# Kernel tuning notes

Hardware: AMD Instinct MI355X
Metric: run time of the kernel (lower is better)

The kernel has to match this reference:

```python
import jax, jax.numpy as jnp
import numpy as np

SEQ, D_IN, D_OUT = 8192, 1024, 1024


def setup_inputs() -> dict:
    key = jax.random.key(0)
    kx, kq, kk, kv = jax.random.split(key, 4)
    x = jax.random.normal(kx, (SEQ, D_IN), dtype=jnp.float32)
    # original uses torch.rand (uniform [0,1)) for parameter init
    WQ = jax.random.uniform(kq, (D_IN, D_OUT), dtype=jnp.float32)
    WK = jax.random.uniform(kk, (D_IN, D_OUT), dtype=jnp.float32)
    WV = jax.random.uniform(kv, (D_IN, D_OUT), dtype=jnp.float32)
    return {"x": x, "WQ": WQ, "WK": WK, "WV": WV}


def reference(x, WQ, WK, WV):
    # [seq, d_out] projections
    q = x @ WQ
    k = x @ WK
    v = x @ WV
    # [seq, seq] raw attention scores
    attn_score = q @ k.T
    # NOTE: source module computes softmax(attn_score/sqrt(d)) into attn_wt
    # but then multiplies the RAW scores by values (attn_score @ values).
    # attn_wt is dead code w.r.t. the output, so it is omitted here.
    context_vct = attn_score @ v  # [seq, d_out]
    return context_vct
```

## Files before the change

kernel.cpp:

```cpp
#include <hip/hip_runtime.h>
#include <hip/hip_bf16.h>
#include <stdint.h>
#include <stddef.h>

#define SEQ  8192
#define DIN  1024
#define DOUT 1024

typedef __hip_bfloat16 bf16;
typedef short bf16x8 __attribute__((ext_vector_type(8)));
typedef float f32x4  __attribute__((ext_vector_type(4)));

#define GLOAD_LDS16(gptr, lptr)                                                     \
  __builtin_amdgcn_global_load_lds(                                                 \
      (const __attribute__((address_space(1))) void*)(gptr),                        \
      (__attribute__((address_space(3))) void*)(lptr), 16, 0, 0)

__device__ inline void store_out(float* p, float v) { *p = v; }
__device__ inline void store_out(bf16* p, float v) { *p = __float2bfloat16(v); }
__device__ inline short bfbits(float f) { bf16 b = __float2bfloat16(f); return *(short*)&b; }
__device__ inline float bf2f(short u) {
  unsigned v = ((unsigned)(unsigned short)u) << 16;
  return __uint_as_float(v);
}

template <typename OutT>
__device__ __forceinline__ void gemm128_body(
    const bf16* __restrict__ A, const bf16* __restrict__ B, OutT* __restrict__ C,
    int bx, int by, int K, int lda, int ldb, int ldc, bf16* As, bf16* Bs)
{
  const int lane = threadIdx.x & 63;
  const int wave = threadIdx.x >> 6;
  const int m0 = by * 128, n0 = bx * 128;

  const int sR = lane >> 3;
  const int sC = (lane & 7) ^ sR;
  const bf16* gA = A + (size_t)(m0 + sR) * lda + sC * 8;
  const bf16* gB = B + (size_t)(n0 + sR) * ldb + sC * 8;

  f32x4 acc[4][4];
#pragma unroll
  for (int i = 0; i < 4; ++i)
#pragma unroll
    for (int j = 0; j < 4; ++j)
      acc[i][j] = (f32x4){0.f, 0.f, 0.f, 0.f};

  const int wr = wave >> 1, wc = wave & 1;
  const int mW = wr * 64, nW = wc * 64;
  const int fragRow = lane & 15;
  const int quad = lane >> 4;

  auto stage = [&](int kt, int buf) {
    bf16* dA = As + buf * (128 * 64);
    bf16* dB = Bs + buf * (128 * 64);
#pragma unroll
    for (int t = 0; t < 4; ++t) {
      const int R = (t * 4 + wave) * 8;
      GLOAD_LDS16(gA + (size_t)R * lda + kt, &dA[R * 64]);
      GLOAD_LDS16(gB + (size_t)R * ldb + kt, &dB[R * 64]);
    }
  };

  const int nT = K >> 6;
  stage(0, 0);
  for (int kt = 0; kt < nT; ++kt) {
    const int buf = kt & 1;
    if (kt + 1 < nT) {
      stage((kt + 1) << 6, buf ^ 1);
      asm volatile("s_waitcnt vmcnt(8)" ::: "memory");
    } else {
      asm volatile("s_waitcnt vmcnt(0)" ::: "memory");
    }
    asm volatile("s_barrier" ::: "memory");

    const bf16* Ab = As + buf * (128 * 64);
    const bf16* Bb = Bs + buf * (128 * 64);
    bf16x8 afr[2][4], bfr[2][4];
#pragma unroll
    for (int s = 0; s < 2; ++s) {
      const int cw = s * 4 + quad;
#pragma unroll
      for (int i = 0; i < 4; ++i) {
        const int ra = mW + i * 16 + fragRow;
        afr[s][i] = *(const bf16x8*)&Ab[ra * 64 + ((cw ^ (ra & 7)) << 3)];
        const int rb = nW + i * 16 + fragRow;
        bfr[s][i] = *(const bf16x8*)&Bb[rb * 64 + ((cw ^ (rb & 7)) << 3)];
      }
    }
    asm volatile("s_waitcnt lgkmcnt(0)" ::: "memory");
    asm volatile("s_barrier" ::: "memory");

#pragma unroll
    for (int s = 0; s < 2; ++s)
#pragma unroll
      for (int i = 0; i < 4; ++i)
#pragma unroll
        for (int j = 0; j < 4; ++j)
          acc[i][j] = __builtin_amdgcn_mfma_f32_16x16x32_bf16(afr[s][i], bfr[s][j], acc[i][j], 0, 0, 0);
  }

  const int cCol  = lane & 15;
  const int cRow4 = quad * 4;
#pragma unroll
  for (int i = 0; i < 4; ++i)
#pragma unroll
    for (int j = 0; j < 4; ++j) {
      const int row = m0 + mW + i * 16 + cRow4;
      const int col = n0 + nW + j * 16 + cCol;
#pragma unroll
      for (int r = 0; r < 4; ++r)
        store_out(&C[(size_t)(row + r) * ldc + col], acc[i][j][r]);
    }
}

template <typename OutT>
__device__ __forceinline__ void gemm64_body(
    const bf16* __restrict__ A, const bf16* __restrict__ B, OutT* __restrict__ C,
    int bx, int by, int K, int lda, int ldb, int ldc, bf16* As, bf16* Bs)
{
  const int lane = threadIdx.x & 63;
  const int wave = threadIdx.x >> 6;
  const int m0 = by * 64, n0 = bx * 64;

  const int sR = lane >> 3;
  const int sC = (lane & 7) ^ sR;
  const bf16* gA = A + (size_t)(m0 + sR) * lda + sC * 8;
  const bf16* gB = B + (size_t)(n0 + sR) * ldb + sC * 8;

  f32x4 acc[2][2];
#pragma unroll
  for (int i = 0; i < 2; ++i)
#pragma unroll
    for (int j = 0; j < 2; ++j)
      acc[i][j] = (f32x4){0.f, 0.f, 0.f, 0.f};

  const int wr = wave >> 1, wc = wave & 1;
  const int mW = wr * 32, nW = wc * 32;
  const int fragRow = lane & 15;
  const int quad = lane >> 4;

  auto stage = [&](int kt, int buf) {
    bf16* dA = As + buf * (64 * 64);
    bf16* dB = Bs + buf * (64 * 64);
#pragma unroll
    for (int t = 0; t < 2; ++t) {
      const int R = (t * 4 + wave) * 8;
      GLOAD_LDS16(gA + (size_t)R * lda + kt, &dA[R * 64]);
      GLOAD_LDS16(gB + (size_t)R * ldb + kt, &dB[R * 64]);
    }
  };

  const int nT = K >> 6;
  stage(0, 0);
  for (int kt = 0; kt < nT; ++kt) {
    const int buf = kt & 1;
    if (kt + 1 < nT) {
      stage((kt + 1) << 6, buf ^ 1);
      asm volatile("s_waitcnt vmcnt(4)" ::: "memory");
    } else {
      asm volatile("s_waitcnt vmcnt(0)" ::: "memory");
    }
    asm volatile("s_barrier" ::: "memory");

    const bf16* Ab = As + buf * (64 * 64);
    const bf16* Bb = Bs + buf * (64 * 64);
    bf16x8 afr[2][2], bfr[2][2];
#pragma unroll
    for (int s = 0; s < 2; ++s) {
      const int cw = s * 4 + quad;
#pragma unroll
      for (int i = 0; i < 2; ++i) {
        const int ra = mW + i * 16 + fragRow;
        afr[s][i] = *(const bf16x8*)&Ab[ra * 64 + ((cw ^ (ra & 7)) << 3)];
        const int rb = nW + i * 16 + fragRow;
        bfr[s][i] = *(const bf16x8*)&Bb[rb * 64 + ((cw ^ (rb & 7)) << 3)];
      }
    }
    asm volatile("s_waitcnt lgkmcnt(0)" ::: "memory");
    asm volatile("s_barrier" ::: "memory");

#pragma unroll
    for (int s = 0; s < 2; ++s)
#pragma unroll
      for (int i = 0; i < 2; ++i)
#pragma unroll
        for (int j = 0; j < 2; ++j)
          acc[i][j] = __builtin_amdgcn_mfma_f32_16x16x32_bf16(afr[s][i], bfr[s][j], acc[i][j], 0, 0, 0);
  }

  const int cCol  = lane & 15;
  const int cRow4 = quad * 4;
#pragma unroll
  for (int i = 0; i < 2; ++i)
#pragma unroll
    for (int j = 0; j < 2; ++j) {
      const int row = m0 + mW + i * 16 + cRow4;
      const int col = n0 + nW + j * 16 + cCol;
#pragma unroll
      for (int r = 0; r < 4; ++r)
        store_out(&C[(size_t)(row + r) * ldc + col], acc[i][j][r]);
    }
}

__global__ __launch_bounds__(256) void g_p1(
    const bf16* __restrict__ xT, const bf16* __restrict__ WQb,
    const bf16* __restrict__ WKb, bf16* __restrict__ part, bf16* __restrict__ P1)
{
  __shared__ bf16 sm[4 * 128 * 64];
  const int b = blockIdx.x;
  if (b < 512) {
    const int z = b & 7;
    const int r = b >> 3;
    const bf16* Az = xT + (size_t)z * 1024;
    gemm128_body<bf16>(Az, Az, part + ((size_t)z << 20),
                       r & 7, r >> 3, 1024, 8192, 8192, 1024,
                       sm, sm + 2 * 128 * 64);
  } else {
    const int p = b - 512;
    gemm64_body<bf16>(WQb, WKb, P1, p & 15, p >> 4, 1024, 1024, 1024, 1024,
                      sm, sm + 2 * 64 * 64);
  }
}

__global__ __launch_bounds__(256) void gemm128_f32(
    const bf16* __restrict__ A, const bf16* __restrict__ B, float* __restrict__ C,
    int K, int lda, int ldb, int ldc)
{
  __shared__ bf16 sm[4 * 128 * 64];
  const int id = blockIdx.x;
  const int by = ((id & 7) << 3) | ((id >> 3) & 7);
  const int bx = id >> 6;
  gemm128_body<float>(A, B, C, bx, by, K, lda, ldb, ldc, sm, sm + 2 * 128 * 64);
}

__global__ __launch_bounds__(256) void gemm64_bf(
    const bf16* __restrict__ A, const bf16* __restrict__ B, bf16* __restrict__ C,
    int K, int lda, int ldb, int ldc)
{
  __shared__ bf16 sm[4 * 64 * 64];
  gemm64_body<bf16>(A, B, C, blockIdx.x, blockIdx.y, K, lda, ldb, ldc,
                    sm, sm + 2 * 64 * 64);
}

__global__ __launch_bounds__(256) void prep_all(
    const float* __restrict__ x, const float* __restrict__ WQ,
    const float* __restrict__ WK, const float* __restrict__ WV,
    bf16* __restrict__ xb, bf16* __restrict__ xTb,
    bf16* __restrict__ WQb, bf16* __restrict__ WKb, bf16* __restrict__ WVTb)
{
  __shared__ bf16 t[128][68];
  int b = blockIdx.x;

  if (b < 5120) {
    const size_t i = ((size_t)b * 256 + threadIdx.x) * 8;
    const float* src; bf16* dst;
    if (i < 8388608)      { src = x  + i;           dst = xb  + i; }
    else if (i < 9437184) { src = WQ + (i - 8388608); dst = WQb + (i - 8388608); }
    else                  { src = WK + (i - 9437184); dst = WKb + (i - 9437184); }
    const float4 f0 = *(const float4*)src;
    const float4 f1 = *(const float4*)(src + 4);
    bf16x8 o;
    o[0] = bfbits(f0.x); o[1] = bfbits(f0.y); o[2] = bfbits(f0.z); o[3] = bfbits(f0.w);
    o[4] = bfbits(f1.x); o[5] = bfbits(f1.y); o[6] = bfbits(f1.z); o[7] = bfbits(f1.w);
    *(bf16x8*)dst = o;
    return;
  }

  b -= 5120;
  const float* src; bf16* dst; int ldOut, tr, tc;
  if (b < 1024) { src = x;  dst = xTb;  ldOut = SEQ; tr = b >> 4; tc = b & 15; }
  else { b -= 1024; src = WV; dst = WVTb; ldOut = DIN; tr = b >> 4; tc = b & 15; }
  const int r0 = tr * 128, c0 = tc * 64;

#pragma unroll
  for (int p = 0; p < 8; ++p) {
    const int q = threadIdx.x + p * 256;
    const int r = q >> 4, c4 = (q & 15) * 4;
    const float4 f = *(const float4*)&src[(size_t)(r0 + r) * DIN + c0 + c4];
    short4 s4;
    s4.x = bfbits(f.x); s4.y = bfbits(f.y); s4.z = bfbits(f.z); s4.w = bfbits(f.w);
    *(short4*)&t[r][c4] = s4;
  }
  __syncthreads();

#pragma unroll
  for (int p = 0; p < 4; ++p) {
    const int h = threadIdx.x + p * 256;
    const int c = h >> 4, seg = h & 15;
    bf16x8 o;
#pragma unroll
    for (int i = 0; i < 8; ++i)
      o[i] = *(const short*)&t[seg * 8 + i][c];
    *(bf16x8*)&dst[(size_t)(c0 + c) * ldOut + r0 + seg * 8] = o;
  }
}

__global__ void reduce8(const bf16* __restrict__ part, bf16* __restrict__ out, int S)
{
  const int i = blockIdx.x * blockDim.x + threadIdx.x;
  const size_t base = (size_t)i * 8;
  float s[8] = {0.f, 0.f, 0.f, 0.f, 0.f, 0.f, 0.f, 0.f};
  for (int z = 0; z < S; ++z) {
    bf16x8 v = *(const bf16x8*)&part[((size_t)z << 20) + base];
#pragma unroll
    for (int r = 0; r < 8; ++r) s[r] += bf2f(v[r]);
  }
  bf16x8 o;
#pragma unroll
  for (int r = 0; r < 8; ++r) o[r] = bfbits(s[r]);
  *(bf16x8*)&out[base] = o;
}

extern "C" void kernel_launch(void* const* d_in, const int* in_sizes, int n_in,
                              void* d_out, int out_size, void* d_ws, size_t ws_size,
                              hipStream_t stream)
{
  const float* x  = (const float*)d_in[0];
  const float* WQ = (const float*)d_in[1];
  const float* WK = (const float*)d_in[2];
  const float* WV = (const float*)d_in[3];
  float* out = (float*)d_out;

  char* ws = (char*)d_ws;
  size_t off = 0;
  auto alloc = [&](size_t bytes) -> void* {
    void* p = ws + off;
    off += (bytes + 255) & ~(size_t)255;
    return p;
  };

  const size_t xBytes = (size_t)SEQ * DIN * sizeof(bf16);
  const size_t wBytes = (size_t)DIN * DOUT * sizeof(bf16);
  const int S = 8;

  bf16* xb   = (bf16*)alloc(xBytes);
  bf16* xTb  = (bf16*)alloc(xBytes);
  bf16* WQb  = (bf16*)alloc(wBytes);
  bf16* WKb  = (bf16*)alloc(wBytes);
  bf16* WVTb = (bf16*)alloc(wBytes);
  bf16* Gb   = (bf16*)alloc(wBytes);
  bf16* P1b  = (bf16*)alloc(wBytes);
  bf16* Utb  = (bf16*)alloc(wBytes);
  bf16* WpTb = (bf16*)alloc(wBytes);
  bf16* part = (bf16*)alloc((size_t)S * wBytes);

  prep_all<<<dim3(6272), 256, 0, stream>>>(x, WQ, WK, WV, xb, xTb, WQb, WKb, WVTb);

  g_p1<<<dim3(768), 256, 0, stream>>>(xTb, WQb, WKb, part, P1b);

  reduce8<<<dim3(512), 256, 0, stream>>>(part, Gb, S);

  gemm64_bf<<<dim3(16, 16), 256, 0, stream>>>(WVTb, Gb, Utb, 1024, 1024, 1024, 1024);
  gemm64_bf<<<dim3(16, 16), 256, 0, stream>>>(Utb, P1b, WpTb, 1024, 1024, 1024, 1024);

  gemm128_f32<<<dim3(512), 256, 0, stream>>>(xb, WpTb, out, 1024, 1024, 1024, DOUT);
}
```

Baseline: 164.5 us.

## Fuse WQ·WKᵀ product into prep kernel and emit xb during transpose

The separate elementwise bf16 conversion pass over x, WQ and WK is removed. The row-major bf16 copy of x is now written inside the transpose blocks that already read x. The WQ·WKᵀ product (P1) is computed directly from fp32 inputs by new blocks in the prep kernel, converting to bf16 while staging into shared memory. The x^T x partial GEMM kernel no longer carries the P1 blocks. This cuts an extra full read of x and an intermediate write and read of the weights. In exchange, the new P1 path has no async loads or double buffering, and the xb stores are short4-sized and less coalesced.

```diff
diff --git a/kernel.cpp b/kernel.cpp
--- a/kernel.cpp
+++ b/kernel.cpp
@@ -202,24 +202,107 @@
     }
 }
 
-__global__ __launch_bounds__(256) void g_p1(
-    const bf16* __restrict__ xT, const bf16* __restrict__ WQb,
-    const bf16* __restrict__ WKb, bf16* __restrict__ part, bf16* __restrict__ P1)
+__device__ __forceinline__ void p1_body(
+    const float* __restrict__ A, const float* __restrict__ B, bf16* __restrict__ C,
+    int bx, int by, bf16* As, bf16* Bs)
+{
+  const int tid  = threadIdx.x;
+  const int lane = tid & 63;
+  const int wave = tid >> 6;
+  const int m0 = by * 64, n0 = bx * 64;
+
+  const int sRow = tid >> 2;
+  const int sJ   = (tid & 3) << 1;
+
+  f32x4 acc[2][2];
+#pragma unroll
+  for (int i = 0; i < 2; ++i)
+#pragma unroll
+    for (int j = 0; j < 2; ++j)
+      acc[i][j] = (f32x4){0.f, 0.f, 0.f, 0.f};
+
+  const int wr = wave >> 1, wc = wave & 1;
+  const int mW = wr * 32, nW = wc * 32;
+  const int fragRow = lane & 15;
+  const int quad = lane >> 4;
+
+  const float* gA = A + (size_t)(m0 + sRow) * 1024;
+  const float* gB = B + (size_t)(n0 + sRow) * 1024;
+
+  for (int kt = 0; kt < 16; ++kt) {
+    const int k0 = kt << 6;
+    float4 ra[2][2], rb[2][2];
+#pragma unroll
+    for (int u = 0; u < 2; ++u) {
+      const int c = k0 + ((sJ + u) << 3);
+      ra[u][0] = *(const float4*)&gA[c];
+      ra[u][1] = *(const float4*)&gA[c + 4];
+      rb[u][0] = *(const float4*)&gB[c];
+      rb[u][1] = *(const float4*)&gB[c + 4];
+    }
+    __syncthreads();
+#pragma unroll
+    for (int u = 0; u < 2; ++u) {
+      bf16x8 pa, pb;
+      pa[0] = bfbits(ra[u][0].x); pa[1] = bfbits(ra[u][0].y);
+      pa[2] = bfbits(ra[u][0].z); pa[3] = bfbits(ra[u][0].w);
+      pa[4] = bfbits(ra[u][1].x); pa[5] = bfbits(ra[u][1].y);
+      pa[6] = bfbits(ra[u][1].z); pa[7] = bfbits(ra[u][1].w);
+      pb[0] = bfbits(rb[u][0].x); pb[1] = bfbits(rb[u][0].y);
+      pb[2] = bfbits(rb[u][0].z); pb[3] = bfbits(rb[u][0].w);
+      pb[4] = bfbits(rb[u][1].x); pb[5] = bfbits(rb[u][1].y);
+      pb[6] = bfbits(rb[u][1].z); pb[7] = bfbits(rb[u][1].w);
+      *(bf16x8*)&As[sRow * 72 + (sJ + u) * 8] = pa;
+      *(bf16x8*)&Bs[sRow * 72 + (sJ + u) * 8] = pb;
+    }
+    __syncthreads();
+
+    bf16x8 afr[2][2], bfr[2][2];
+#pragma unroll
+    for (int s = 0; s < 2; ++s) {
+      const int cw = s * 4 + quad;
+#pragma unroll
+      for (int i = 0; i < 2; ++i) {
+        const int rr = mW + i * 16 + fragRow;
+        afr[s][i] = *(const bf16x8*)&As[rr * 72 + cw * 8];
+        const int cc = nW + i * 16 + fragRow;
+        bfr[s][i] = *(const bf16x8*)&Bs[cc * 72 + cw * 8];
+      }
+    }
+#pragma unroll
+    for (int s = 0; s < 2; ++s)
+#pragma unroll
+      for (int i = 0; i < 2; ++i)
+#pragma unroll
+        for (int j = 0; j < 2; ++j)
+          acc[i][j] = __builtin_amdgcn_mfma_f32_16x16x32_bf16(afr[s][i], bfr[s][j], acc[i][j], 0, 0, 0);
+  }
+
+  const int cCol  = lane & 15;
+  const int cRow4 = quad * 4;
+#pragma unroll
+  for (int i = 0; i < 2; ++i)
+#pragma unroll
+    for (int j = 0; j < 2; ++j) {
+      const int row = m0 + mW + i * 16 + cRow4;
+      const int col = n0 + nW + j * 16 + cCol;
+#pragma unroll
+      for (int r = 0; r < 4; ++r)
+        store_out(&C[(size_t)(row + r) * 1024 + col], acc[i][j][r]);
+    }
+}
+
+__global__ __launch_bounds__(256) void g_G(
+    const bf16* __restrict__ xT, bf16* __restrict__ part)
 {
   __shared__ bf16 sm[4 * 128 * 64];
   const int b = blockIdx.x;
-  if (b < 512) {
-    const int z = b & 7;
-    const int r = b >> 3;
-    const bf16* Az = xT + (size_t)z * 1024;
-    gemm128_body<bf16>(Az, Az, part + ((size_t)z << 20),
-                       r & 7, r >> 3, 1024, 8192, 8192, 1024,
-                       sm, sm + 2 * 128 * 64);
-  } else {
-    const int p = b - 512;
-    gemm64_body<bf16>(WQb, WKb, P1, p & 15, p >> 4, 1024, 1024, 1024, 1024,
-                      sm, sm + 2 * 64 * 64);
-  }
+  const int z = b & 7;
+  const int r = b >> 3;
+  const bf16* Az = xT + (size_t)z * 1024;
+  gemm128_body<bf16>(Az, Az, part + ((size_t)z << 20),
+                     r & 7, r >> 3, 1024, 8192, 8192, 1024,
+                     sm, sm + 2 * 128 * 64);
 }
 
 __global__ __launch_bounds__(256) void gemm128_f32(
@@ -246,30 +329,21 @@
     const float* __restrict__ x, const float* __restrict__ WQ,
     const float* __restrict__ WK, const float* __restrict__ WV,
     bf16* __restrict__ xb, bf16* __restrict__ xTb,
-    bf16* __restrict__ WQb, bf16* __restrict__ WKb, bf16* __restrict__ WVTb)
-{
-  __shared__ bf16 t[128][68];
+    bf16* __restrict__ WVTb, bf16* __restrict__ P1)
+{
+  __shared__ __align__(16) bf16 sm[2 * 64 * 72];
   int b = blockIdx.x;
 
-  if (b < 5120) {
-    const size_t i = ((size_t)b * 256 + threadIdx.x) * 8;
-    const float* src; bf16* dst;
-    if (i < 8388608)      { src = x  + i;           dst = xb  + i; }
-    else if (i < 9437184) { src = WQ + (i - 8388608); dst = WQb + (i - 8388608); }
-    else                  { src = WK + (i - 9437184); dst = WKb + (i - 9437184); }
-    const float4 f0 = *(const float4*)src;
-    const float4 f1 = *(const float4*)(src + 4);
-    bf16x8 o;
-    o[0] = bfbits(f0.x); o[1] = bfbits(f0.y); o[2] = bfbits(f0.z); o[3] = bfbits(f0.w);
-    o[4] = bfbits(f1.x); o[5] = bfbits(f1.y); o[6] = bfbits(f1.z); o[7] = bfbits(f1.w);
-    *(bf16x8*)dst = o;
+  if (b < 256) {
+    p1_body(WQ, WK, P1, b & 15, b >> 4, sm, sm + 64 * 72);
     return;
   }
-
-  b -= 5120;
-  const float* src; bf16* dst; int ldOut, tr, tc;
-  if (b < 1024) { src = x;  dst = xTb;  ldOut = SEQ; tr = b >> 4; tc = b & 15; }
-  else { b -= 1024; src = WV; dst = WVTb; ldOut = DIN; tr = b >> 4; tc = b & 15; }
+  b -= 256;
+
+  bf16 (*t)[68] = (bf16(*)[68])sm;
+  const float* src; bf16* dst; int ldOut, tr, tc; bool isX;
+  if (b < 1024) { src = x;  dst = xTb;  ldOut = SEQ; tr = b >> 4; tc = b & 15; isX = true; }
+  else { b -= 1024; src = WV; dst = WVTb; ldOut = DIN; tr = b >> 4; tc = b & 15; isX = false; }
   const int r0 = tr * 128, c0 = tc * 64;
 
 #pragma unroll
@@ -280,6 +354,7 @@
     short4 s4;
     s4.x = bfbits(f.x); s4.y = bfbits(f.y); s4.z = bfbits(f.z); s4.w = bfbits(f.w);
     *(short4*)&t[r][c4] = s4;
+    if (isX) *(short4*)&xb[(size_t)(r0 + r) * DIN + c0 + c4] = s4;
   }
   __syncthreads();
 
@@ -335,8 +410,6 @@
 
   bf16* xb   = (bf16*)alloc(xBytes);
   bf16* xTb  = (bf16*)alloc(xBytes);
-  bf16* WQb  = (bf16*)alloc(wBytes);
-  bf16* WKb  = (bf16*)alloc(wBytes);
   bf16* WVTb = (bf16*)alloc(wBytes);
   bf16* Gb   = (bf16*)alloc(wBytes);
   bf16* P1b  = (bf16*)alloc(wBytes);
@@ -344,9 +417,9 @@
   bf16* WpTb = (bf16*)alloc(wBytes);
   bf16* part = (bf16*)alloc((size_t)S * wBytes);
 
-  prep_all<<<dim3(6272), 256, 0, stream>>>(x, WQ, WK, WV, xb, xTb, WQb, WKb, WVTb);
-
-  g_p1<<<dim3(768), 256, 0, stream>>>(xTb, WQb, WKb, part, P1b);
+  prep_all<<<dim3(1408), 256, 0, stream>>>(x, WQ, WK, WV, xb, xTb, WVTb, P1b);
+
+  g_G<<<dim3(512), 256, 0, stream>>>(xTb, part);
 
   reduce8<<<dim3(512), 256, 0, stream>>>(part, Gb, S);
 
```

Measured after the change: 168.2 us. +2.2%, slower.

## Exploit Gram matrix symmetry and fuse x conversion into transpose pass

Applied to the files above, without the earlier changes.

The Gram matrix G = x^T x is now computed only for the 36 upper-triangular 128x128 tiles, with split-K partials reduced in a new kernel that also writes the mirrored transpose tile through swizzled LDS. The x bf16 cast is folded into the transposing prep pass so x is read once instead of twice, and the P1 and Ut GEMMs are merged into one launch. This cuts G-GEMM work by nearly half and removes a launch. The cost is a serialized reduction over only 36 blocks and a triangular grid of 288 blocks, which may underfill the GPU.

```diff
diff --git a/kernel.cpp b/kernel.cpp
--- a/kernel.cpp
+++ b/kernel.cpp
@@ -22,6 +22,12 @@
 __device__ inline float bf2f(short u) {
   unsigned v = ((unsigned)(unsigned short)u) << 16;
   return __uint_as_float(v);
+}
+
+__device__ inline void tri_map(int t, int& ti, int& tj) {
+  int a = 0, rem = t;
+  while (rem >= 8 - a) { rem -= 8 - a; ++a; }
+  ti = a; tj = a + rem;
 }
 
 template <typename OutT>
@@ -202,24 +208,89 @@
     }
 }
 
-__global__ __launch_bounds__(256) void g_p1(
-    const bf16* __restrict__ xT, const bf16* __restrict__ WQb,
-    const bf16* __restrict__ WKb, bf16* __restrict__ part, bf16* __restrict__ P1)
+__global__ __launch_bounds__(256) void g_G(
+    const bf16* __restrict__ xT, bf16* __restrict__ part)
 {
   __shared__ bf16 sm[4 * 128 * 64];
   const int b = blockIdx.x;
-  if (b < 512) {
-    const int z = b & 7;
-    const int r = b >> 3;
-    const bf16* Az = xT + (size_t)z * 1024;
-    gemm128_body<bf16>(Az, Az, part + ((size_t)z << 20),
-                       r & 7, r >> 3, 1024, 8192, 8192, 1024,
-                       sm, sm + 2 * 128 * 64);
+  const int z = b & 7;
+  const int t = b >> 3;
+  int ti, tj; tri_map(t, ti, tj);
+  const bf16* Az = xT + (size_t)z * 1024;
+  gemm128_body<bf16>(Az + (size_t)ti * 128 * 8192,
+                     Az + (size_t)tj * 128 * 8192,
+                     part + ((size_t)(z * 36 + t)) * 16384,
+                     0, 0, 1024, 8192, 8192, 128,
+                     sm, sm + 2 * 128 * 64);
+}
+
+__global__ __launch_bounds__(256) void reduceT(
+    const bf16* __restrict__ part, bf16* __restrict__ G)
+{
+  __shared__ bf16 red[128 * 128];
+  const int t = blockIdx.x;
+  int ti, tj; tri_map(t, ti, tj);
+  const int tid = threadIdx.x;
+  const size_t base = (size_t)t * 16384;
+  const bool diag = (ti == tj);
+
+#pragma unroll
+  for (int it = 0; it < 8; ++it) {
+    const int flat = it * 256 + tid;
+    const int row = flat >> 4, chunk = flat & 15;
+    float a[8] = {0.f, 0.f, 0.f, 0.f, 0.f, 0.f, 0.f, 0.f};
+    for (int z = 0; z < 8; ++z) {
+      bf16x8 v = *(const bf16x8*)&part[(size_t)z * 36 * 16384 + base + row * 128 + chunk * 8];
+#pragma unroll
+      for (int r = 0; r < 8; ++r) a[r] += bf2f(v[r]);
+    }
+    bf16x8 o;
+#pragma unroll
+    for (int r = 0; r < 8; ++r) o[r] = bfbits(a[r]);
+    *(bf16x8*)&G[(size_t)(ti * 128 + row) * 1024 + tj * 128 + chunk * 8] = o;
+    if (!diag)
+      *(bf16x8*)&red[row * 128 + ((chunk ^ (row >> 3)) << 3)] = o;
+  }
+  if (diag) return;
+  __syncthreads();
+
+#pragma unroll
+  for (int it = 0; it < 8; ++it) {
+    const int flat = it * 256 + tid;
+    const int c = flat >> 4, seg = flat & 15;
+    const int swz = ((((c >> 3) ^ seg)) << 3) + (c & 7);
+    bf16x8 o;
+#pragma unroll
+    for (int i = 0; i < 8; ++i)
+      o[i] = *(const short*)&red[(seg * 8 + i) * 128 + swz];
+    *(bf16x8*)&G[(size_t)(tj * 128 + c) * 1024 + ti * 128 + seg * 8] = o;
+  }
+}
+
+__global__ __launch_bounds__(256) void g_ut_p1(
+    const bf16* __restrict__ WVT, const bf16* __restrict__ G,
+    const bf16* __restrict__ WQb, const bf16* __restrict__ WKb,
+    bf16* __restrict__ Ut, bf16* __restrict__ P1)
+{
+  __shared__ bf16 sm[4 * 64 * 64];
+  int b = blockIdx.x;
+  if (b < 256) {
+    gemm64_body<bf16>(WQb, WKb, P1, b & 15, b >> 4, 1024, 1024, 1024, 1024,
+                      sm, sm + 2 * 64 * 64);
   } else {
-    const int p = b - 512;
-    gemm64_body<bf16>(WQb, WKb, P1, p & 15, p >> 4, 1024, 1024, 1024, 1024,
+    b -= 256;
+    gemm64_body<bf16>(WVT, G, Ut, b & 15, b >> 4, 1024, 1024, 1024, 1024,
                       sm, sm + 2 * 64 * 64);
   }
+}
+
+__global__ __launch_bounds__(256) void gemm64_bf(
+    const bf16* __restrict__ A, const bf16* __restrict__ B, bf16* __restrict__ C,
+    int K, int lda, int ldb, int ldc)
+{
+  __shared__ bf16 sm[4 * 64 * 64];
+  gemm64_body<bf16>(A, B, C, blockIdx.x, blockIdx.y, K, lda, ldb, ldc,
+                    sm, sm + 2 * 64 * 64);
 }
 
 __global__ __launch_bounds__(256) void gemm128_f32(
@@ -233,15 +304,6 @@
   gemm128_body<float>(A, B, C, bx, by, K, lda, ldb, ldc, sm, sm + 2 * 128 * 64);
 }
 
-__global__ __launch_bounds__(256) void gemm64_bf(
-    const bf16* __restrict__ A, const bf16* __restrict__ B, bf16* __restrict__ C,
-    int K, int lda, int ldb, int ldc)
-{
-  __shared__ bf16 sm[4 * 64 * 64];
-  gemm64_body<bf16>(A, B, C, blockIdx.x, blockIdx.y, K, lda, ldb, ldc,
-                    sm, sm + 2 * 64 * 64);
-}
-
 __global__ __launch_bounds__(256) void prep_all(
     const float* __restrict__ x, const float* __restrict__ WQ,
     const float* __restrict__ WK, const float* __restrict__ WV,
@@ -251,12 +313,11 @@
   __shared__ bf16 t[128][68];
   int b = blockIdx.x;
 
-  if (b < 5120) {
-    const size_t i = ((size_t)b * 256 + threadIdx.x) * 8;
+  if (b >= 1152) {
+    const size_t i = ((size_t)(b - 1152) * 256 + threadIdx.x) * 8;
     const float* src; bf16* dst;
-    if (i < 8388608)      { src = x  + i;           dst = xb  + i; }
-    else if (i < 9437184) { src = WQ + (i - 8388608); dst = WQb + (i - 8388608); }
-    else                  { src = WK + (i - 9437184); dst = WKb + (i - 9437184); }
+    if (i < 1048576) { src = WQ + i;             dst = WQb + i; }
+    else             { src = WK + (i - 1048576); dst = WKb + (i - 1048576); }
     const float4 f0 = *(const float4*)src;
     const float4 f1 = *(const float4*)(src + 4);
     bf16x8 o;
@@ -266,10 +327,9 @@
     return;
   }
 
-  b -= 5120;
-  const float* src; bf16* dst; int ldOut, tr, tc;
-  if (b < 1024) { src = x;  dst = xTb;  ldOut = SEQ; tr = b >> 4; tc = b & 15; }
-  else { b -= 1024; src = WV; dst = WVTb; ldOut = DIN; tr = b >> 4; tc = b & 15; }
+  const float* src; bf16* dst; int ldOut, tr, tc; bool isX;
+  if (b < 1024) { src = x;  dst = xTb;  ldOut = SEQ; tr = b >> 4; tc = b & 15; isX = true; }
+  else { b -= 1024; src = WV; dst = WVTb; ldOut = DIN; tr = b >> 4; tc = b & 15; isX = false; }
   const int r0 = tr * 128, c0 = tc * 64;
 
 #pragma unroll
@@ -280,6 +340,7 @@
     short4 s4;
     s4.x = bfbits(f.x); s4.y = bfbits(f.y); s4.z = bfbits(f.z); s4.w = bfbits(f.w);
     *(short4*)&t[r][c4] = s4;
+    if (isX) *(short4*)&xb[(size_t)(r0 + r) * DIN + c0 + c4] = s4;
   }
   __syncthreads();
 
@@ -293,22 +354,6 @@
       o[i] = *(const short*)&t[seg * 8 + i][c];
     *(bf16x8*)&dst[(size_t)(c0 + c) * ldOut + r0 + seg * 8] = o;
   }
-}
-
-__global__ void reduce8(const bf16* __restrict__ part, bf16* __restrict__ out, int S)
-{
-  const int i = blockIdx.x * blockDim.x + threadIdx.x;
-  const size_t base = (size_t)i * 8;
-  float s[8] = {0.f, 0.f, 0.f, 0.f, 0.f, 0.f, 0.f, 0.f};
-  for (int z = 0; z < S; ++z) {
-    bf16x8 v = *(const bf16x8*)&part[((size_t)z << 20) + base];
-#pragma unroll
-    for (int r = 0; r < 8; ++r) s[r] += bf2f(v[r]);
-  }
-  bf16x8 o;
-#pragma unroll
-  for (int r = 0; r < 8; ++r) o[r] = bfbits(s[r]);
-  *(bf16x8*)&out[base] = o;
 }
 
 extern "C" void kernel_launch(void* const* d_in, const int* in_sizes, int n_in,
@@ -331,7 +376,6 @@
 
   const size_t xBytes = (size_t)SEQ * DIN * sizeof(bf16);
   const size_t wBytes = (size_t)DIN * DOUT * sizeof(bf16);
-  const int S = 8;
 
   bf16* xb   = (bf16*)alloc(xBytes);
   bf16* xTb  = (bf16*)alloc(xBytes);
@@ -342,15 +386,16 @@
   bf16* P1b  = (bf16*)alloc(wBytes);
   bf16* Utb  = (bf16*)alloc(wBytes);
   bf16* WpTb = (bf16*)alloc(wBytes);
-  bf16* part = (bf16*)alloc((size_t)S * wBytes);
-
-  prep_all<<<dim3(6272), 256, 0, stream>>>(x, WQ, WK, WV, xb, xTb, WQb, WKb, WVTb);
-
-  g_p1<<<dim3(768), 256, 0, stream>>>(xTb, WQb, WKb, part, P1b);
-
-  reduce8<<<dim3(512), 256, 0, stream>>>(part, Gb, S);
-
-  gemm64_bf<<<dim3(16, 16), 256, 0, stream>>>(WVTb, Gb, Utb, 1024, 1024, 1024, 1024);
+  bf16* part = (bf16*)alloc((size_t)8 * 36 * 16384 * sizeof(bf16));
+
+  prep_all<<<dim3(2176), 256, 0, stream>>>(x, WQ, WK, WV, xb, xTb, WQb, WKb, WVTb);
+
+  g_G<<<dim3(288), 256, 0, stream>>>(xTb, part);
+
+  reduceT<<<dim3(36), 256, 0, stream>>>(part, Gb);
+
+  g_ut_p1<<<dim3(512), 256, 0, stream>>>(WVTb, Gb, WQb, WKb, Utb, P1b);
+
   gemm64_bf<<<dim3(16, 16), 256, 0, stream>>>(Utb, P1b, WpTb, 1024, 1024, 1024, 1024);
 
   gemm128_f32<<<dim3(512), 256, 0, stream>>>(xb, WpTb, out, 1024, 1024, 1024, DOUT);
```

Measured after the change: 161.0 us. -2.2%, faster.
